# Kernel tuning notes

Measured on AMD Instinct MI355X. Metric: run time of the kernel, lower is better.

## Reference

```python
import jax, jax.numpy as jnp
import numpy as np

GRID = 16
K = 2
NW = (GRID - K + 1) ** 2  # 225 sliding 2x2 windows on the 16x16 grid


def _make_mask():
    idx = np.arange(GRID * GRID).reshape(GRID, GRID)
    wins = np.stack([idx[i:i + K, j:j + K].ravel()
                     for i in range(GRID - K + 1) for j in range(GRID - K + 1)])
    m = np.zeros((NW, GRID * GRID), np.float32)
    m[np.arange(NW)[:, None], wins] = 1.0
    return jnp.asarray(m)

MASK = _make_mask()          # [225, 256] window -> covered cells
MASK_COUNT = MASK.sum(0)     # windows covering each cell
BN_SCALE = np.float32(1.0 / np.sqrt(1.0 + 1e-5))  # eval BN, running mean=0 var=1


def _adapter(x, w1, w2):
    return jax.nn.relu(jax.nn.relu(x @ w1.T) @ w2.T)


def _bn(x, g, b):
    return x * (g * BN_SCALE) + b


def _head(x, w1, b1, g2, be2, w2, b2, g3, be3, w3, b3):
    x = _bn(jax.nn.relu(x @ w1.T + b1), g2, be2)
    x = _bn(jax.nn.relu(x @ w2.T + b2), g3, be3)
    return jax.nn.sigmoid(x @ w3.T + b3)[:, 0]


def setup_inputs() -> dict:
    B, L, P, D, R, S = 64, 3, 225, 640, 1800, 240
    key = jax.random.key(0)
    ks = jax.random.split(key, 16)
    n = lambda k, s, sc=1.0: jax.random.normal(k, s, jnp.float32) * sc
    te = n(ks[3], (2, D)); te = te / jnp.linalg.norm(te, axis=-1, keepdims=True)
    pr = n(ks[5], (L, R, D)); pr = pr / jnp.linalg.norm(pr, axis=-1, keepdims=True)
    w = 0.05
    return dict(
        image=n(ks[0], (B, 3, S, S)),
        image_embeds=n(ks[1], (B, D)),
        patch_embeds=n(ks[2], (L, B, P, D)),
        text_embeds=te,
        image_embeds_ref=n(ks[4], (1, D)),
        patch_embeds_ref=pr,
        a_w1=n(ks[6], (160, D), w), a_w2=n(ks[7], (D, 160), w),
        r_w1=n(ks[8], (128, D), w), r_b1=jnp.zeros((128,)),
        r_g2=jnp.ones((128,)), r_be2=jnp.zeros((128,)),
        r_w2=n(ks[9], (64, 128), w), r_b2=jnp.zeros((64,)),
        r_g3=jnp.ones((64,)), r_be3=jnp.zeros((64,)),
        r_w3=n(ks[10], (1, 64), w), r_b3=jnp.zeros((1,)),
        h_w1=n(ks[11], (128, P), w), h_b1=jnp.zeros((128,)),
        h_g2=jnp.ones((128,)), h_be2=jnp.zeros((128,)),
        h_w2=n(ks[12], (64, 128), w), h_b2=jnp.zeros((64,)),
        h_g3=jnp.ones((64,)), h_be3=jnp.zeros((64,)),
        h_w3=n(ks[13], (1, 64), w), h_b3=jnp.zeros((1,)),
    )


def reference(image, image_embeds, patch_embeds, text_embeds, image_embeds_ref,
              patch_embeds_ref, a_w1, a_w2,
              r_w1, r_b1, r_g2, r_be2, r_w2, r_b2, r_g3, r_be3, r_w3, r_b3,
              h_w1, h_b1, h_g2, h_be2, h_w2, h_b2, h_g3, h_be3, h_w3, h_b3):
    pe = patch_embeds / jnp.linalg.norm(patch_embeds, axis=-1, keepdims=True)
    nie = image_embeds / jnp.linalg.norm(image_embeds, axis=-1, keepdims=True)
    text_score = jax.nn.softmax(100.0 * nie @ text_embeds.T, axis=-1)[:, 1]
    # kNN-style min-distance over reference patches: [L,B,P,R]
    sim = jnp.einsum('lbpd,lrd->lbpr', pe, patch_embeds_ref)
    patch_ref_map = ((1.0 - sim).min(axis=3) / 2.0).mean(axis=0)  # [B,P]
    fg_score = patch_ref_map.max(axis=1)
    diff = image_embeds_ref - _adapter(image_embeds, a_w1, a_w2)
    img_ref_score = _head(diff, r_w1, r_b1, r_g2, r_be2, r_w2, r_b2, r_g3, r_be3, r_w3, r_b3)
    holistic = (text_score + img_ref_score)[:, None] + patch_ref_map  # [B,225]
    hl_score = _head(holistic, h_w1, h_b1, h_g2, h_be2, h_w2, h_b2, h_g3, h_be3, h_w3, h_b3)
    final_score = (hl_score + fg_score) / 2.0
    # harmonic aggregation of window scores onto the 16x16 grid
    heat = (MASK_COUNT / ((1.0 / holistic) @ MASK)).reshape(-1, GRID, GRID)
    hmap = jax.image.resize(heat, (heat.shape[0], image.shape[2], image.shape[3]), 'bilinear')
    return final_score, hmap
```

## Files before the change

kernel.cpp:

```cpp
#include <hip/hip_runtime.h>
#include <stdint.h>
#include <math.h>

#define L_DIM 3
#define B_DIM 64
#define P_DIM 225
#define D_DIM 640
#define R_DIM 1800
#define S_DIM 240
#define M_TOT 14400
#define M_PAD 14592
#define N_PAD 2048
#define MT 57
#define NT 8
#define KT 10
#define BNSCALE 0.99999500003749981f

typedef __bf16 bf16x8 __attribute__((ext_vector_type(8)));
typedef float f32x4 __attribute__((ext_vector_type(4)));

__device__ __forceinline__ unsigned short f2bf(float f) {
    union { float f; unsigned u; } v; v.f = f;
    unsigned u = v.u;
    unsigned r = (u + 0x7FFFu + ((u >> 16) & 1u)) >> 16;
    return (unsigned short)r;
}

__global__ __launch_bounds__(256)
void k_convert(const float* __restrict__ pe, const float* __restrict__ per,
               unsigned short* __restrict__ abf, unsigned short* __restrict__ rbf,
               float* __restrict__ rnorm)
{
    const int AROWS = L_DIM * M_PAD;
    int wid = (blockIdx.x * 256 + threadIdx.x) >> 6;
    int lane = threadIdx.x & 63;
    const ushort4 z4 = {0, 0, 0, 0};
    if (wid < AROWS) {
        int l = wid / M_PAD, r = wid - l * M_PAD;
        unsigned short* dst = abf + (size_t)wid * D_DIM;
        if (r < M_TOT) {
            const float4* src = (const float4*)(pe + ((size_t)l * M_TOT + r) * D_DIM);
            float ss = 0.f;
            #pragma unroll
            for (int it = 0; it < 3; ++it) {
                int idx = it * 64 + lane;
                if (idx < 160) {
                    float4 v = src[idx];
                    ss += v.x * v.x + v.y * v.y + v.z * v.z + v.w * v.w;
                    ushort4 o;
                    o.x = f2bf(v.x); o.y = f2bf(v.y); o.z = f2bf(v.z); o.w = f2bf(v.w);
                    *(ushort4*)(dst + idx * 4) = o;
                }
            }
            #pragma unroll
            for (int m = 32; m; m >>= 1) ss += __shfl_xor(ss, m);
            if (lane == 0) rnorm[l * M_TOT + r] = rsqrtf(ss);
        } else {
            #pragma unroll
            for (int it = 0; it < 3; ++it) {
                int idx = it * 64 + lane;
                if (idx < 160) *(ushort4*)(dst + idx * 4) = z4;
            }
        }
    } else {
        int w2 = wid - AROWS;
        int l = w2 / N_PAD, r = w2 - l * N_PAD;
        unsigned short* dst = rbf + (size_t)w2 * D_DIM;
        if (r < R_DIM) {
            const float4* src = (const float4*)(per + ((size_t)l * R_DIM + r) * D_DIM);
            #pragma unroll
            for (int it = 0; it < 3; ++it) {
                int idx = it * 64 + lane;
                if (idx < 160) {
                    float4 v = src[idx];
                    ushort4 o;
                    o.x = f2bf(v.x); o.y = f2bf(v.y); o.z = f2bf(v.z); o.w = f2bf(v.w);
                    *(ushort4*)(dst + idx * 4) = o;
                }
            }
        } else {
            #pragma unroll
            for (int it = 0; it < 3; ++it) {
                int idx = it * 64 + lane;
                if (idx < 160) *(ushort4*)(dst + idx * 4) = z4;
            }
        }
    }
}

#define MFMA(A, B, C) __builtin_amdgcn_mfma_f32_16x16x32_bf16((A), (B), (C), 0, 0, 0)
#define GLL(SRC, DSTOFF)                                                     \
    __builtin_amdgcn_global_load_lds(                                        \
        (const __attribute__((address_space(1))) void*)(SRC),               \
        (__attribute__((address_space(3))) void*)(lds + (DSTOFF)), 16, 0, 0)

#define RD_Q(D, Q, BASE) do {                                                \
    D[0] = *(const bf16x8*)(lds + (BASE) + (brow0 + (Q) * 32) * 64 + sw0);   \
    D[1] = *(const bf16x8*)(lds + (BASE) + (brow0 + (Q) * 32) * 64 + sw1);   \
    D[2] = *(const bf16x8*)(lds + (BASE) + (brow0 + (Q) * 32 + 16) * 64 + sw0); \
    D[3] = *(const bf16x8*)(lds + (BASE) + (brow0 + (Q) * 32 + 16) * 64 + sw1); \
} while (0)

#define RD_A(BASE) do { _Pragma("unroll")                                    \
    for (int mi = 0; mi < 4; ++mi) {                                         \
        a[mi][0] = *(const bf16x8*)(lds + (BASE) + (arow0 + mi * 16) * 64 + sw0); \
        a[mi][1] = *(const bf16x8*)(lds + (BASE) + (arow0 + mi * 16) * 64 + sw1); \
    } } while (0)

#define MM(NJB, BQ) do { _Pragma("unroll")                                   \
    for (int mi = 0; mi < 4; ++mi) {                                         \
        acc[mi][NJB]     = MFMA(a[mi][0], BQ[0], acc[mi][NJB]);              \
        acc[mi][NJB]     = MFMA(a[mi][1], BQ[1], acc[mi][NJB]);              \
        acc[mi][NJB + 1] = MFMA(a[mi][0], BQ[2], acc[mi][NJB + 1]);          \
        acc[mi][NJB + 1] = MFMA(a[mi][1], BQ[3], acc[mi][NJB + 1]);          \
    } } while (0)

__global__ __launch_bounds__(512, 1)
void k_gemm_max(const unsigned short* __restrict__ abf,
                const unsigned short* __restrict__ rbf,
                float* __restrict__ pmax)
{
    __shared__ unsigned short lds[65536];
    __shared__ float red[2][256];

    int bid = blockIdx.x;
    int v = (bid & 7) * 171 + (bid >> 3);
    int l = v / (MT * NT);
    int rem = v - l * (MT * NT);
    int mt = rem >> 3;
    int nt = rem & 7;

    int tid = threadIdx.x;
    int wid = tid >> 6, lane = tid & 63;
    int wm = wid >> 1;
    int wn = wid & 1;
    int lane15 = lane & 15, lg = lane >> 4;
    int sA = lane15 & 7;
    int sw0 = ((lg) ^ sA) << 3;
    int sw1 = ((4 + lg) ^ sA) << 3;
    int arow0 = wm * 64 + lane15;
    int brow0 = wn * 128 + lane15;

    int rowc = lane >> 3;
    int scol = ((lane & 7) ^ rowc) << 3;
    const unsigned short* gA = abf + (size_t)(l * M_PAD + mt * 256) * D_DIM;
    const unsigned short* gB = rbf + (size_t)(l * N_PAD + nt * 256) * D_DIM;
    int chA0 = wid, chA1 = 8 + wid, chA2 = 16 + wid, chA3 = 24 + wid;
    int chB0 = (wid < 4) ? (0 + wid) : (12 + wid);
    int chB1 = (wid < 4) ? (4 + wid) : (16 + wid);
    int chB2 = (wid < 4) ? (8 + wid) : (20 + wid);
    int chB3 = (wid < 4) ? (12 + wid) : (24 + wid);
    const unsigned short* pA0 = gA + (size_t)(chA0 * 8 + rowc) * D_DIM + scol;
    const unsigned short* pA1 = gA + (size_t)(chA1 * 8 + rowc) * D_DIM + scol;
    const unsigned short* pA2 = gA + (size_t)(chA2 * 8 + rowc) * D_DIM + scol;
    const unsigned short* pA3 = gA + (size_t)(chA3 * 8 + rowc) * D_DIM + scol;
    const unsigned short* pB0 = gB + (size_t)(chB0 * 8 + rowc) * D_DIM + scol;
    const unsigned short* pB1 = gB + (size_t)(chB1 * 8 + rowc) * D_DIM + scol;
    const unsigned short* pB2 = gB + (size_t)(chB2 * 8 + rowc) * D_DIM + scol;
    const unsigned short* pB3 = gB + (size_t)(chB3 * 8 + rowc) * D_DIM + scol;

    f32x4 acc[4][8];
    #pragma unroll
    for (int mi = 0; mi < 4; ++mi)
        #pragma unroll
        for (int nj = 0; nj < 8; ++nj)
            acc[mi][nj] = f32x4{0.f, 0.f, 0.f, 0.f};

    GLL(pA0, chA0 * 512); GLL(pA1, chA1 * 512);
    GLL(pA2, chA2 * 512); GLL(pA3, chA3 * 512);
    GLL(pB0, 32768 + chB0 * 512); GLL(pB1, 32768 + chB1 * 512);
    GLL(pB2, 32768 + chB2 * 512); GLL(pB3, 32768 + chB3 * 512);
    asm volatile("s_waitcnt vmcnt(2)" ::: "memory");
    __builtin_amdgcn_s_barrier();

    int buf = 0;
    for (int kt = 0; kt < KT - 1; ++kt) {
        int ob = buf ^ 1;
        int aB = buf * 16384;
        int bB = 32768 + buf * 16384;
        int oaB = ob * 16384;
        int obB = 32768 + ob * 16384;
        int koff = (kt + 1) * 64;

        bf16x8 a[4][2];
        {
            RD_A(aB);
            bf16x8 q0[4], q1[4];
            RD_Q(q0, 0, bB); RD_Q(q1, 1, bB);
            GLL(pA0 + koff, oaB + chA0 * 512); GLL(pA1 + koff, oaB + chA1 * 512);
            GLL(pA2 + koff, oaB + chA2 * 512); GLL(pA3 + koff, oaB + chA3 * 512);
            asm volatile("s_waitcnt vmcnt(4)" ::: "memory");
            __builtin_amdgcn_s_barrier();
            __builtin_amdgcn_s_setprio(1);
            MM(0, q0); MM(2, q1);
            __builtin_amdgcn_s_setprio(0);
        }
        {
            bf16x8 q2[4], q3[4];
            RD_Q(q2, 2, bB); RD_Q(q3, 3, bB);
            GLL(pB0 + koff, obB + chB0 * 512); GLL(pB1 + koff, obB + chB1 * 512);
            GLL(pB2 + koff, obB + chB2 * 512); GLL(pB3 + koff, obB + chB3 * 512);
            asm volatile("s_waitcnt vmcnt(2)" ::: "memory");
            __builtin_amdgcn_s_barrier();
            __builtin_amdgcn_s_setprio(1);
            MM(4, q2); MM(6, q3);
            __builtin_amdgcn_s_setprio(0);
        }
        buf = ob;
    }

    {
        int aB = buf * 16384;
        int bB = 32768 + buf * 16384;
        bf16x8 a[4][2];
        RD_A(aB);
        bf16x8 q0[4], q1[4];
        RD_Q(q0, 0, bB); RD_Q(q1, 1, bB);
        asm volatile("s_waitcnt vmcnt(0)" ::: "memory");
        __builtin_amdgcn_s_barrier();
        __builtin_amdgcn_s_setprio(1);
        MM(0, q0); MM(2, q1);
        __builtin_amdgcn_s_setprio(0);
        bf16x8 q2[4], q3[4];
        RD_Q(q2, 2, bB); RD_Q(q3, 3, bB);
        __builtin_amdgcn_s_setprio(1);
        MM(4, q2); MM(6, q3);
        __builtin_amdgcn_s_setprio(0);
    }

    __syncthreads();

    int colbase = nt * 256 + wn * 128 + lane15;
    #pragma unroll
    for (int mi = 0; mi < 4; ++mi) {
        float t[4] = {-__builtin_inff(), -__builtin_inff(),
                      -__builtin_inff(), -__builtin_inff()};
        #pragma unroll
        for (int nj = 0; nj < 8; ++nj) {
            if (colbase + nj * 16 < R_DIM) {
                #pragma unroll
                for (int r = 0; r < 4; ++r) t[r] = fmaxf(t[r], acc[mi][nj][r]);
            }
        }
        #pragma unroll
        for (int m = 1; m <= 8; m <<= 1) {
            #pragma unroll
            for (int r = 0; r < 4; ++r) t[r] = fmaxf(t[r], __shfl_xor(t[r], m));
        }
        if (lane15 == 0) {
            int rb = wm * 64 + mi * 16 + lg * 4;
            #pragma unroll
            for (int r = 0; r < 4; ++r) red[wn][rb + r] = t[r];
        }
    }
    __syncthreads();
    if (tid < 256) {
        float vmx = fmaxf(red[0][tid], red[1][tid]);
        pmax[((size_t)l * NT + nt) * M_PAD + mt * 256 + tid] = vmx;
    }
}

__device__ __forceinline__ float block_sum8(float v, volatile float* scratch) {
    #pragma unroll
    for (int m = 32; m; m >>= 1) v += __shfl_xor(v, m);
    int w = threadIdx.x >> 6;
    __syncthreads();
    if ((threadIdx.x & 63) == 0) scratch[w] = v;
    __syncthreads();
    float r = 0.f;
    #pragma unroll
    for (int i = 0; i < 8; ++i) r += scratch[i];
    return r;
}
__device__ __forceinline__ float block_max8(float v, volatile float* scratch) {
    #pragma unroll
    for (int m = 32; m; m >>= 1) v = fmaxf(v, __shfl_xor(v, m));
    int w = threadIdx.x >> 6;
    __syncthreads();
    if ((threadIdx.x & 63) == 0) scratch[w] = v;
    __syncthreads();
    float r = scratch[0];
    #pragma unroll
    for (int i = 1; i < 8; ++i) r = fmaxf(r, scratch[i]);
    return r;
}

__global__ __launch_bounds__(512)
void k_small(const float* __restrict__ ie, const float* __restrict__ te,
             const float* __restrict__ ier,
             const float* __restrict__ a_w1, const float* __restrict__ a_w2,
             const float* __restrict__ r_w1, const float* __restrict__ r_b1,
             const float* __restrict__ r_g2, const float* __restrict__ r_be2,
             const float* __restrict__ r_w2, const float* __restrict__ r_b2,
             const float* __restrict__ r_g3, const float* __restrict__ r_be3,
             const float* __restrict__ r_w3, const float* __restrict__ r_b3,
             const float* __restrict__ h_w1, const float* __restrict__ h_b1,
             const float* __restrict__ h_g2, const float* __restrict__ h_be2,
             const float* __restrict__ h_w2, const float* __restrict__ h_b2,
             const float* __restrict__ h_g3, const float* __restrict__ h_be3,
             const float* __restrict__ h_w3, const float* __restrict__ h_b3,
             const float* __restrict__ pmax, const float* __restrict__ rnorm,
             float* __restrict__ out_score, float* __restrict__ outh)
{
    int b = blockIdx.x, tid = threadIdx.x;
    __shared__ float x[D_DIM];
    __shared__ float h1[160];
    __shared__ float dif[D_DIM];
    __shared__ float z1[128];
    __shared__ float z2[64];
    __shared__ float hol[P_DIM];
    __shared__ float rcp[P_DIM];
    __shared__ float heatl[256];
    __shared__ float scratch[8];

    for (int i = tid; i < D_DIM; i += 512) x[i] = ie[b * D_DIM + i];
    __syncthreads();

    float ss = 0.f, d0 = 0.f, d1 = 0.f;
    for (int i = tid; i < D_DIM; i += 512) {
        float v = x[i];
        ss += v * v;
        d0 += v * te[i];
        d1 += v * te[D_DIM + i];
    }
    float ssum = block_sum8(ss, scratch);
    float dd0 = block_sum8(d0, scratch);
    float dd1 = block_sum8(d1, scratch);
    float tscore = 1.f / (1.f + expf(100.f * rsqrtf(ssum) * (dd0 - dd1)));

    for (int o = tid; o < 160; o += 512) {
        const float* w = a_w1 + (size_t)o * D_DIM;
        float s0 = 0, s1 = 0, s2 = 0, s3 = 0;
        for (int d = 0; d < D_DIM; d += 4) {
            s0 += x[d] * w[d]; s1 += x[d + 1] * w[d + 1];
            s2 += x[d + 2] * w[d + 2]; s3 += x[d + 3] * w[d + 3];
        }
        h1[o] = fmaxf((s0 + s1) + (s2 + s3), 0.f);
    }
    __syncthreads();
    for (int d = tid; d < D_DIM; d += 512) {
        const float* w = a_w2 + (size_t)d * 160;
        float s0 = 0, s1 = 0, s2 = 0, s3 = 0;
        for (int o = 0; o < 160; o += 4) {
            s0 += h1[o] * w[o]; s1 += h1[o + 1] * w[o + 1];
            s2 += h1[o + 2] * w[o + 2]; s3 += h1[o + 3] * w[o + 3];
        }
        dif[d] = ier[d] - fmaxf((s0 + s1) + (s2 + s3), 0.f);
    }
    __syncthreads();

    for (int o = tid; o < 128; o += 512) {
        const float* w = r_w1 + (size_t)o * D_DIM;
        float s0 = 0, s1 = 0, s2 = 0, s3 = 0;
        for (int d = 0; d < D_DIM; d += 4) {
            s0 += dif[d] * w[d]; s1 += dif[d + 1] * w[d + 1];
            s2 += dif[d + 2] * w[d + 2]; s3 += dif[d + 3] * w[d + 3];
        }
        float s = (s0 + s1) + (s2 + s3) + r_b1[o];
        z1[o] = fmaxf(s, 0.f) * (r_g2[o] * BNSCALE) + r_be2[o];
    }
    __syncthreads();
    for (int o = tid; o < 64; o += 512) {
        const float* w = r_w2 + (size_t)o * 128;
        float s = r_b2[o];
        for (int d = 0; d < 128; ++d) s += z1[d] * w[d];
        z2[o] = fmaxf(s, 0.f) * (r_g3[o] * BNSCALE) + r_be3[o];
    }
    __syncthreads();
    float sp = (tid < 64) ? z2[tid] * r_w3[tid] : 0.f;
    float irs = 1.f / (1.f + expf(-(block_sum8(sp, scratch) + r_b3[0])));

    float fgp = -__builtin_inff();
    float base = tscore + irs;
    for (int p = tid; p < P_DIM; p += 512) {
        int r = b * P_DIM + p;
        float s = 0.f;
        #pragma unroll
        for (int l = 0; l < L_DIM; ++l) {
            float m = -__builtin_inff();
            #pragma unroll
            for (int t = 0; t < NT; ++t)
                m = fmaxf(m, pmax[((size_t)l * NT + t) * M_PAD + r]);
            s += m * rnorm[l * M_TOT + r];
        }
        float pv = (3.0f - s) / 6.0f;
        fgp = fmaxf(fgp, pv);
        float h = base + pv;
        hol[p] = h;
        rcp[p] = 1.f / h;
    }
    float fg = block_max8(fgp, scratch);

    for (int o = tid; o < 128; o += 512) {
        const float* w = h_w1 + (size_t)o * P_DIM;
        float s = h_b1[o];
        for (int d = 0; d < P_DIM; ++d) s += hol[d] * w[d];
        z1[o] = fmaxf(s, 0.f) * (h_g2[o] * BNSCALE) + h_be2[o];
    }
    __syncthreads();
    for (int o = tid; o < 64; o += 512) {
        const float* w = h_w2 + (size_t)o * 128;
        float s = h_b2[o];
        for (int d = 0; d < 128; ++d) s += z1[d] * w[d];
        z2[o] = fmaxf(s, 0.f) * (h_g3[o] * BNSCALE) + h_be3[o];
    }
    __syncthreads();
    float sp2 = (tid < 64) ? z2[tid] * h_w3[tid] : 0.f;
    float hl_in = block_sum8(sp2, scratch) + h_b3[0];
    if (tid == 0) {
        float hl = 1.f / (1.f + expf(-hl_in));
        out_score[b] = (hl + fg) * 0.5f;
    }

    if (tid < 256) {
        int r = tid >> 4, c = tid & 15;
        float s = 0.f, cnt = 0.f;
        #pragma unroll
        for (int di = -1; di <= 0; ++di) {
            int i = r + di;
            if (i < 0 || i > 14) continue;
            #pragma unroll
            for (int dj = -1; dj <= 0; ++dj) {
                int j = c + dj;
                if (j < 0 || j > 14) continue;
                s += rcp[i * 15 + j];
                cnt += 1.f;
            }
        }
        heatl[tid] = cnt / s;
    }
    __syncthreads();

    float* dst = outh + (size_t)b * (S_DIM * S_DIM);
    for (int px = tid; px < S_DIM * S_DIM; px += 512) {
        int y = px / S_DIM, xc = px - y * S_DIM;
        float sy = fminf(fmaxf((y - 7) * (1.0f / 15.0f), 0.f), 15.f);
        float sx = fminf(fmaxf((xc - 7) * (1.0f / 15.0f), 0.f), 15.f);
        int y0 = (int)sy, x0 = (int)sx;
        int y1 = min(y0 + 1, 15), x1 = min(x0 + 1, 15);
        float fy = sy - (float)y0, fx = sx - (float)x0;
        float v00 = heatl[y0 * 16 + x0], v01 = heatl[y0 * 16 + x1];
        float v10 = heatl[y1 * 16 + x0], v11 = heatl[y1 * 16 + x1];
        float vv = (1.f - fy) * ((1.f - fx) * v00 + fx * v01)
                 + fy * ((1.f - fx) * v10 + fx * v11);
        dst[px] = vv;
    }
}

extern "C" void kernel_launch(void* const* d_in, const int* in_sizes, int n_in,
                              void* d_out, int out_size, void* d_ws, size_t ws_size,
                              hipStream_t stream)
{
    (void)in_sizes; (void)n_in; (void)out_size; (void)ws_size;
    const float* image_embeds = (const float*)d_in[1];
    const float* patch_embeds = (const float*)d_in[2];
    const float* text_embeds  = (const float*)d_in[3];
    const float* ier          = (const float*)d_in[4];
    const float* per          = (const float*)d_in[5];
    const float* a_w1 = (const float*)d_in[6];
    const float* a_w2 = (const float*)d_in[7];
    const float* r_w1 = (const float*)d_in[8];
    const float* r_b1 = (const float*)d_in[9];
    const float* r_g2 = (const float*)d_in[10];
    const float* r_be2 = (const float*)d_in[11];
    const float* r_w2 = (const float*)d_in[12];
    const float* r_b2 = (const float*)d_in[13];
    const float* r_g3 = (const float*)d_in[14];
    const float* r_be3 = (const float*)d_in[15];
    const float* r_w3 = (const float*)d_in[16];
    const float* r_b3 = (const float*)d_in[17];
    const float* h_w1 = (const float*)d_in[18];
    const float* h_b1 = (const float*)d_in[19];
    const float* h_g2 = (const float*)d_in[20];
    const float* h_be2 = (const float*)d_in[21];
    const float* h_w2 = (const float*)d_in[22];
    const float* h_b2 = (const float*)d_in[23];
    const float* h_g3 = (const float*)d_in[24];
    const float* h_be3 = (const float*)d_in[25];
    const float* h_w3 = (const float*)d_in[26];
    const float* h_b3 = (const float*)d_in[27];

    char* ws = (char*)d_ws;
    size_t off = 0;
    auto take = [&](size_t bytes) -> void* {
        void* p = ws + off;
        off += (bytes + 255) & ~(size_t)255;
        return p;
    };
    float* rnorm = (float*)take((size_t)L_DIM * M_TOT * 4);
    float* pmax  = (float*)take((size_t)L_DIM * NT * M_PAD * 4);
    unsigned short* abf = (unsigned short*)take((size_t)L_DIM * M_PAD * D_DIM * 2);
    unsigned short* rbf = (unsigned short*)take((size_t)L_DIM * N_PAD * D_DIM * 2);

    float* out_f = (float*)d_out;

    k_convert<<<dim3((L_DIM * M_PAD + L_DIM * N_PAD) / 4), dim3(256), 0, stream>>>(
        patch_embeds, per, abf, rbf, rnorm);
    k_gemm_max<<<dim3(L_DIM * MT * NT), dim3(512), 0, stream>>>(abf, rbf, pmax);
    k_small<<<dim3(B_DIM), dim3(512), 0, stream>>>(image_embeds, text_embeds, ier,
        a_w1, a_w2, r_w1, r_b1, r_g2, r_be2, r_w2, r_b2, r_g3, r_be3, r_w3, r_b3,
        h_w1, h_b1, h_g2, h_be2, h_w2, h_b2, h_g3, h_be3, h_w3, h_b3,
        pmax, rnorm, out_f, out_f + B_DIM);
}
```

Before: 214.6 us.

## Retile similarity GEMM to 128x256 tiles with triple-buffered K=32 pipeline

Restructures the bf16 MFMA GEMM-with-row-max kernel. M tiles shrink from 256 to 128 rows (less padding, more blocks), the K step drops from 64 to 32, and a 3-stage LDS ring with prefetch distance 2 replaces the double buffer, using one barrier per step. LDS use per block falls so launch bounds now allow several blocks per CU, which aims to raise occupancy and hide latency. The cost is lower arithmetic intensity per tile, more loop iterations and barriers, and a new LDS swizzle and wave layout that must still line up with the MFMA operand layout.

```diff
diff --git a/kernel.cpp b/kernel.cpp
--- a/kernel.cpp
+++ b/kernel.cpp
@@ -9,11 +9,11 @@
 #define R_DIM 1800
 #define S_DIM 240
 #define M_TOT 14400
-#define M_PAD 14592
+#define M_PAD 14464
 #define N_PAD 2048
-#define MT 57
+#define MT 113
 #define NT 8
-#define KT 10
+#define KT 20
 #define BNSCALE 0.99999500003749981f
 
 typedef __bf16 bf16x8 __attribute__((ext_vector_type(8)));
@@ -94,37 +94,16 @@
         (const __attribute__((address_space(1))) void*)(SRC),               \
         (__attribute__((address_space(3))) void*)(lds + (DSTOFF)), 16, 0, 0)
 
-#define RD_Q(D, Q, BASE) do {                                                \
-    D[0] = *(const bf16x8*)(lds + (BASE) + (brow0 + (Q) * 32) * 64 + sw0);   \
-    D[1] = *(const bf16x8*)(lds + (BASE) + (brow0 + (Q) * 32) * 64 + sw1);   \
-    D[2] = *(const bf16x8*)(lds + (BASE) + (brow0 + (Q) * 32 + 16) * 64 + sw0); \
-    D[3] = *(const bf16x8*)(lds + (BASE) + (brow0 + (Q) * 32 + 16) * 64 + sw1); \
-} while (0)
-
-#define RD_A(BASE) do { _Pragma("unroll")                                    \
-    for (int mi = 0; mi < 4; ++mi) {                                         \
-        a[mi][0] = *(const bf16x8*)(lds + (BASE) + (arow0 + mi * 16) * 64 + sw0); \
-        a[mi][1] = *(const bf16x8*)(lds + (BASE) + (arow0 + mi * 16) * 64 + sw1); \
-    } } while (0)
-
-#define MM(NJB, BQ) do { _Pragma("unroll")                                   \
-    for (int mi = 0; mi < 4; ++mi) {                                         \
-        acc[mi][NJB]     = MFMA(a[mi][0], BQ[0], acc[mi][NJB]);              \
-        acc[mi][NJB]     = MFMA(a[mi][1], BQ[1], acc[mi][NJB]);              \
-        acc[mi][NJB + 1] = MFMA(a[mi][0], BQ[2], acc[mi][NJB + 1]);          \
-        acc[mi][NJB + 1] = MFMA(a[mi][1], BQ[3], acc[mi][NJB + 1]);          \
-    } } while (0)
-
-__global__ __launch_bounds__(512, 1)
+__global__ __launch_bounds__(512, 4)
 void k_gemm_max(const unsigned short* __restrict__ abf,
                 const unsigned short* __restrict__ rbf,
                 float* __restrict__ pmax)
 {
-    __shared__ unsigned short lds[65536];
-    __shared__ float red[2][256];
+    __shared__ unsigned short lds[36864];
+    __shared__ float red[4][128];
 
     int bid = blockIdx.x;
-    int v = (bid & 7) * 171 + (bid >> 3);
+    int v = (bid & 7) * 339 + (bid >> 3);
     int l = v / (MT * NT);
     int rem = v - l * (MT * NT);
     int mt = rem >> 3;
@@ -132,111 +111,81 @@
 
     int tid = threadIdx.x;
     int wid = tid >> 6, lane = tid & 63;
-    int wm = wid >> 1;
-    int wn = wid & 1;
+    int wm = wid >> 2;
+    int wn = wid & 3;
     int lane15 = lane & 15, lg = lane >> 4;
-    int sA = lane15 & 7;
-    int sw0 = ((lg) ^ sA) << 3;
-    int sw1 = ((4 + lg) ^ sA) << 3;
-    int arow0 = wm * 64 + lane15;
-    int brow0 = wn * 128 + lane15;
-
-    int rowc = lane >> 3;
-    int scol = ((lane & 7) ^ rowc) << 3;
-    const unsigned short* gA = abf + (size_t)(l * M_PAD + mt * 256) * D_DIM;
+
+    int lpr = lane >> 3;
+    int c2  = (lane & 7) ^ lpr;
+    int kc  = c2 & 3;
+    int rsub = lpr * 2 + (c2 >> 2);
+    const unsigned short* gA = abf + (size_t)(l * M_PAD + mt * 128) * D_DIM;
     const unsigned short* gB = rbf + (size_t)(l * N_PAD + nt * 256) * D_DIM;
-    int chA0 = wid, chA1 = 8 + wid, chA2 = 16 + wid, chA3 = 24 + wid;
-    int chB0 = (wid < 4) ? (0 + wid) : (12 + wid);
-    int chB1 = (wid < 4) ? (4 + wid) : (16 + wid);
-    int chB2 = (wid < 4) ? (8 + wid) : (20 + wid);
-    int chB3 = (wid < 4) ? (12 + wid) : (24 + wid);
-    const unsigned short* pA0 = gA + (size_t)(chA0 * 8 + rowc) * D_DIM + scol;
-    const unsigned short* pA1 = gA + (size_t)(chA1 * 8 + rowc) * D_DIM + scol;
-    const unsigned short* pA2 = gA + (size_t)(chA2 * 8 + rowc) * D_DIM + scol;
-    const unsigned short* pA3 = gA + (size_t)(chA3 * 8 + rowc) * D_DIM + scol;
-    const unsigned short* pB0 = gB + (size_t)(chB0 * 8 + rowc) * D_DIM + scol;
-    const unsigned short* pB1 = gB + (size_t)(chB1 * 8 + rowc) * D_DIM + scol;
-    const unsigned short* pB2 = gB + (size_t)(chB2 * 8 + rowc) * D_DIM + scol;
-    const unsigned short* pB3 = gB + (size_t)(chB3 * 8 + rowc) * D_DIM + scol;
-
-    f32x4 acc[4][8];
+    const unsigned short* pA  = gA + (size_t)(wid * 16 + rsub) * D_DIM + kc * 8;
+    const unsigned short* pB0 = gB + (size_t)(wid * 16 + rsub) * D_DIM + kc * 8;
+    const unsigned short* pB1 = gB + (size_t)(wid * 16 + 128 + rsub) * D_DIM + kc * 8;
+
+    int pcom = (((lane15 & 1) << 2) + lg) ^ ((lane15 >> 1) & 7);
+    int aoff = (wm * 32 + (lane15 >> 1)) * 64 + pcom * 8;
+    int boff = (wn * 32 + (lane15 >> 1)) * 64 + pcom * 8;
+
+    f32x4 acc[4][4];
     #pragma unroll
     for (int mi = 0; mi < 4; ++mi)
         #pragma unroll
-        for (int nj = 0; nj < 8; ++nj)
+        for (int nj = 0; nj < 4; ++nj)
             acc[mi][nj] = f32x4{0.f, 0.f, 0.f, 0.f};
 
-    GLL(pA0, chA0 * 512); GLL(pA1, chA1 * 512);
-    GLL(pA2, chA2 * 512); GLL(pA3, chA3 * 512);
-    GLL(pB0, 32768 + chB0 * 512); GLL(pB1, 32768 + chB1 * 512);
-    GLL(pB2, 32768 + chB2 * 512); GLL(pB3, 32768 + chB3 * 512);
-    asm volatile("s_waitcnt vmcnt(2)" ::: "memory");
+    GLL(pA, wid * 512);
+    GLL(pB0, 12288 + wid * 512);
+    GLL(pB1, 12288 + (8 + wid) * 512);
+    GLL(pA + 32, 4096 + wid * 512);
+    GLL(pB0 + 32, 12288 + 8192 + wid * 512);
+    GLL(pB1 + 32, 12288 + 8192 + (8 + wid) * 512);
+    asm volatile("s_waitcnt vmcnt(3)" ::: "memory");
     __builtin_amdgcn_s_barrier();
 
-    int buf = 0;
-    for (int kt = 0; kt < KT - 1; ++kt) {
-        int ob = buf ^ 1;
-        int aB = buf * 16384;
-        int bB = 32768 + buf * 16384;
-        int oaB = ob * 16384;
-        int obB = 32768 + ob * 16384;
-        int koff = (kt + 1) * 64;
-
-        bf16x8 a[4][2];
-        {
-            RD_A(aB);
-            bf16x8 q0[4], q1[4];
-            RD_Q(q0, 0, bB); RD_Q(q1, 1, bB);
-            GLL(pA0 + koff, oaB + chA0 * 512); GLL(pA1 + koff, oaB + chA1 * 512);
-            GLL(pA2 + koff, oaB + chA2 * 512); GLL(pA3 + koff, oaB + chA3 * 512);
-            asm volatile("s_waitcnt vmcnt(4)" ::: "memory");
-            __builtin_amdgcn_s_barrier();
-            __builtin_amdgcn_s_setprio(1);
-            MM(0, q0); MM(2, q1);
-            __builtin_amdgcn_s_setprio(0);
-        }
-        {
-            bf16x8 q2[4], q3[4];
-            RD_Q(q2, 2, bB); RD_Q(q3, 3, bB);
-            GLL(pB0 + koff, obB + chB0 * 512); GLL(pB1 + koff, obB + chB1 * 512);
-            GLL(pB2 + koff, obB + chB2 * 512); GLL(pB3 + koff, obB + chB3 * 512);
-            asm volatile("s_waitcnt vmcnt(2)" ::: "memory");
-            __builtin_amdgcn_s_barrier();
-            __builtin_amdgcn_s_setprio(1);
-            MM(4, q2); MM(6, q3);
-            __builtin_amdgcn_s_setprio(0);
-        }
-        buf = ob;
-    }
-
-    {
-        int aB = buf * 16384;
-        int bB = 32768 + buf * 16384;
-        bf16x8 a[4][2];
-        RD_A(aB);
-        bf16x8 q0[4], q1[4];
-        RD_Q(q0, 0, bB); RD_Q(q1, 1, bB);
-        asm volatile("s_waitcnt vmcnt(0)" ::: "memory");
+    int cur = 0;
+    for (int t = 0; t < KT; ++t) {
+        int wr = cur + 2; if (wr >= 3) wr -= 3;
+        int aB = cur * 4096;
+        int bB = 12288 + cur * 8192;
+
+        bf16x8 a[4], b[4];
+        #pragma unroll
+        for (int mi = 0; mi < 4; ++mi)
+            a[mi] = *(const bf16x8*)(lds + aB + aoff + mi * 512);
+        #pragma unroll
+        for (int nj = 0; nj < 4; ++nj)
+            b[nj] = *(const bf16x8*)(lds + bB + boff + nj * 512);
+
+        int koff = (t + 2 < KT ? t + 2 : KT - 1) * 32;
+        GLL(pA + koff, wr * 4096 + wid * 512);
+        GLL(pB0 + koff, 12288 + wr * 8192 + wid * 512);
+        GLL(pB1 + koff, 12288 + wr * 8192 + (8 + wid) * 512);
+        asm volatile("s_waitcnt vmcnt(3)" ::: "memory");
         __builtin_amdgcn_s_barrier();
+
         __builtin_amdgcn_s_setprio(1);
-        MM(0, q0); MM(2, q1);
+        #pragma unroll
+        for (int mi = 0; mi < 4; ++mi)
+            #pragma unroll
+            for (int nj = 0; nj < 4; ++nj)
+                acc[mi][nj] = MFMA(a[mi], b[nj], acc[mi][nj]);
         __builtin_amdgcn_s_setprio(0);
-        bf16x8 q2[4], q3[4];
-        RD_Q(q2, 2, bB); RD_Q(q3, 3, bB);
-        __builtin_amdgcn_s_setprio(1);
-        MM(4, q2); MM(6, q3);
-        __builtin_amdgcn_s_setprio(0);
-    }
-
-    __syncthreads();
-
-    int colbase = nt * 256 + wn * 128 + lane15;
+
+        cur = (cur == 2) ? 0 : cur + 1;
+    }
+
+    __syncthreads();
+
+    int colbase = nt * 256 + wn * 64 + lane15;
     #pragma unroll
     for (int mi = 0; mi < 4; ++mi) {
         float t[4] = {-__builtin_inff(), -__builtin_inff(),
                       -__builtin_inff(), -__builtin_inff()};
         #pragma unroll
-        for (int nj = 0; nj < 8; ++nj) {
+        for (int nj = 0; nj < 4; ++nj) {
             if (colbase + nj * 16 < R_DIM) {
                 #pragma unroll
                 for (int r = 0; r < 4; ++r) t[r] = fmaxf(t[r], acc[mi][nj][r]);
@@ -254,9 +203,10 @@
         }
     }
     __syncthreads();
-    if (tid < 256) {
-        float vmx = fmaxf(red[0][tid], red[1][tid]);
-        pmax[((size_t)l * NT + nt) * M_PAD + mt * 256 + tid] = vmx;
+    if (tid < 128) {
+        float vmx = fmaxf(fmaxf(red[0][tid], red[1][tid]),
+                          fmaxf(red[2][tid], red[3][tid]));
+        pmax[((size_t)l * NT + nt) * M_PAD + mt * 128 + tid] = vmx;
     }
 }
 
```

After: 221.8 us. 1.03x slower.
